# Performance work log

Hardware: AMD Instinct MI355X
Metric: run time of the kernel (lower is better)

The kernel has to match this reference:

```python
import jax, jax.numpy as jnp
import numpy as np

def setup_inputs() -> dict:
    key = jax.random.key(0)
    k1, k2, k3 = jax.random.split(key, 3)
    shape = (2, 2048, 8, 64)  # [n, l, h, d]
    return {
        "q": jax.random.normal(k1, shape, dtype=jnp.float32),
        "k": jax.random.normal(k2, shape, dtype=jnp.float32),
        "v": jax.random.normal(k3, shape, dtype=jnp.float32),
    }

def reference(q, k, v):
    # QK^T: [n, l, s, h]
    qk = jnp.einsum('nlhd,nshd->nlsh', q, k)
    softmax_temp = 1.0 / (q.shape[3] ** 0.5)
    attn = jax.nn.softmax(softmax_temp * qk, axis=2)
    # weighted values: [n, l, h, d]
    return jnp.einsum('nlsh,nshd->nlhd', attn, v)
```

## Files before the change

kernel.cpp:

```cpp
#include <hip/hip_runtime.h>
#include <hip/hip_bf16.h>
#include <math.h>

typedef float floatx4 __attribute__((ext_vector_type(4)));
typedef __bf16 bf16x8 __attribute__((ext_vector_type(8)));

#define SEQ 2048
#define NH 8
#define DH 64
#define NB 2
#define HEADS (NB * NH)
#define HSTRIDE (SEQ * DH)

__device__ __forceinline__ unsigned short f2bf(float x) {
  union { __bf16 b; unsigned short u; } c;
  c.b = (__bf16)x;
  return c.u;
}

__global__ __launch_bounds__(256)
void cvt_kv(const float* __restrict__ k, const float* __restrict__ v,
            unsigned short* __restrict__ kb, unsigned short* __restrict__ vb) {
  __shared__ unsigned short Ts[64][68];
  const int tid  = threadIdx.x;
  const int bx   = blockIdx.x;
  const int ts   = bx & 31;
  const int head = bx >> 5;
  const int n = head >> 3, h = head & 7;

  #pragma unroll
  for (int i = 0; i < 4; ++i) {
    int id = i * 256 + tid;
    int s  = id >> 4;
    int c4 = (id & 15) * 4;
    size_t g = ((size_t)((n * SEQ + ts * 64 + s) * NH + h)) * DH + c4;
    float4 x = *(const float4*)(k + g);
    ushort4 y;
    y.x = f2bf(x.x); y.y = f2bf(x.y); y.z = f2bf(x.z); y.w = f2bf(x.w);
    *(ushort4*)(kb + ((size_t)head * SEQ + ts * 64 + s) * DH + c4) = y;
    float4 xv = *(const float4*)(v + g);
    ushort4 yv;
    yv.x = f2bf(xv.x); yv.y = f2bf(xv.y); yv.z = f2bf(xv.z); yv.w = f2bf(xv.w);
    *(ushort4*)&Ts[s][c4] = yv;
  }
  __syncthreads();
  const int d = tid >> 2;
  const int j = tid & 3;
  size_t ob = ((size_t)head * DH + d) * SEQ + ts * 64 + j * 16;
  #pragma unroll
  for (int c = 0; c < 4; ++c) {
    ushort4 y;
    y.x = Ts[j * 16 + c * 4 + 0][d];
    y.y = Ts[j * 16 + c * 4 + 1][d];
    y.z = Ts[j * 16 + c * 4 + 2][d];
    y.w = Ts[j * 16 + c * 4 + 3][d];
    *(ushort4*)(vb + ob + c * 4) = y;
  }
}

#define SMEM_BYTES 51456

__global__ __launch_bounds__(256, 2)
void attn(const float* __restrict__ q, const unsigned short* __restrict__ kb,
          const unsigned short* __restrict__ vt, float* __restrict__ out) {
  __shared__ __align__(16) char smem[SMEM_BYTES];
  unsigned short (*Pw)[32][72] = (unsigned short (*)[32][72])smem;
  float (*oX)[64][66] = (float (*)[64][66])smem;
  float* lX = (float*)(smem + 3 * 64 * 66 * 4);

  const int tid  = threadIdx.x;
  const int wave = tid >> 6;
  const int lane = tid & 63;
  const int quad = lane >> 4;
  const int l16  = lane & 15;

  const int bx   = blockIdx.x;
  const int head = bx & 15;
  const int qg   = bx >> 4;
  const int n = head >> 3, h = head & 7;

  const unsigned short* kh = kb + (size_t)head * HSTRIDE;
  const unsigned short* vh = vt + (size_t)head * HSTRIDE;

  bf16x8 aq[4][2];
  #pragma unroll
  for (int msub = 0; msub < 4; ++msub)
    #pragma unroll
    for (int f = 0; f < 2; ++f) {
      const float* src = q + ((size_t)((n * SEQ + qg * 64 + msub * 16 + l16) * NH + h)) * DH
                         + f * 32 + quad * 8;
      float4 x0 = *(const float4*)src;
      float4 x1 = *(const float4*)(src + 4);
      union { unsigned short us[8]; bf16x8 v8; } u;
      u.us[0] = f2bf(x0.x); u.us[1] = f2bf(x0.y); u.us[2] = f2bf(x0.z); u.us[3] = f2bf(x0.w);
      u.us[4] = f2bf(x1.x); u.us[5] = f2bf(x1.y); u.us[6] = f2bf(x1.z); u.us[7] = f2bf(x1.w);
      aq[msub][f] = u.v8;
    }

  floatx4 o[4][4];
  float lsum[4][4];
  #pragma unroll
  for (int msub = 0; msub < 4; ++msub) {
    #pragma unroll
    for (int t = 0; t < 4; ++t) o[msub][t] = floatx4{0.f, 0.f, 0.f, 0.f};
    #pragma unroll
    for (int r = 0; r < 4; ++r) lsum[msub][r] = 0.f;
  }

  const float S = 0.125f * 1.4426950408889634f;
  const float C = 12.0f;

  for (int it = 0; it < 8; ++it) {
    const int kbase = (wave * 8 + it) * 64;

    bf16x8 bk[4][2];
    #pragma unroll
    for (int t = 0; t < 4; ++t)
      #pragma unroll
      for (int f = 0; f < 2; ++f)
        bk[t][f] = *(const bf16x8*)(kh + (size_t)(kbase + t * 16 + l16) * DH + f * 32 + quad * 8);
    bf16x8 bv[2][4];
    #pragma unroll
    for (int half = 0; half < 2; ++half)
      #pragma unroll
      for (int t = 0; t < 4; ++t)
        bv[half][t] = *(const bf16x8*)(vh + (size_t)(t * 16 + l16) * SEQ + kbase + half * 32 + quad * 8);

    floatx4 acc[4][4];
    #pragma unroll
    for (int msub = 0; msub < 4; ++msub)
      #pragma unroll
      for (int t = 0; t < 4; ++t) {
        acc[msub][t] = floatx4{0.f, 0.f, 0.f, 0.f};
        #pragma unroll
        for (int f = 0; f < 2; ++f)
          acc[msub][t] = __builtin_amdgcn_mfma_f32_16x16x32_bf16(aq[msub][f], bk[t][f], acc[msub][t], 0, 0, 0);
      }

    #pragma unroll
    for (int mp = 0; mp < 2; ++mp) {
      #pragma unroll
      for (int mi = 0; mi < 2; ++mi) {
        const int msub = mp * 2 + mi;
        #pragma unroll
        for (int t = 0; t < 4; ++t)
          #pragma unroll
          for (int r = 0; r < 4; ++r) {
            float p = __builtin_amdgcn_exp2f(acc[msub][t][r] * S - C);
            lsum[msub][r] += p;
            Pw[wave][mi * 16 + quad * 4 + r][t * 16 + l16] = f2bf(p);
          }
      }
      #pragma unroll
      for (int half = 0; half < 2; ++half)
        #pragma unroll
        for (int mi = 0; mi < 2; ++mi) {
          const int msub = mp * 2 + mi;
          bf16x8 a = *(const bf16x8*)&Pw[wave][mi * 16 + l16][half * 32 + quad * 8];
          #pragma unroll
          for (int t = 0; t < 4; ++t)
            o[msub][t] = __builtin_amdgcn_mfma_f32_16x16x32_bf16(a, bv[half][t], o[msub][t], 0, 0, 0);
        }
    }
  }

  #pragma unroll
  for (int msub = 0; msub < 4; ++msub)
    #pragma unroll
    for (int r = 0; r < 4; ++r) {
      float s = lsum[msub][r];
      #pragma unroll
      for (int d = 1; d < 16; d <<= 1) s += __shfl_xor(s, d, 64);
      lsum[msub][r] = s;
    }

  __syncthreads();
  if (wave != 0) {
    const int w = wave - 1;
    #pragma unroll
    for (int msub = 0; msub < 4; ++msub) {
      #pragma unroll
      for (int t = 0; t < 4; ++t)
        #pragma unroll
        for (int r = 0; r < 4; ++r)
          oX[w][msub * 16 + quad * 4 + r][t * 16 + l16] = o[msub][t][r];
      if (l16 == 0)
        #pragma unroll
        for (int r = 0; r < 4; ++r)
          lX[w * 64 + msub * 16 + quad * 4 + r] = lsum[msub][r];
    }
  }
  __syncthreads();
  if (wave == 0) {
    #pragma unroll
    for (int msub = 0; msub < 4; ++msub)
      #pragma unroll
      for (int r = 0; r < 4; ++r) {
        const int row = msub * 16 + quad * 4 + r;
        float lt = lsum[msub][r] + lX[row] + lX[64 + row] + lX[128 + row];
        float inv = 1.f / lt;
        const int grow = qg * 64 + row;
        size_t ob = ((size_t)((n * SEQ + grow) * NH + h)) * DH + l16;
        #pragma unroll
        for (int t = 0; t < 4; ++t) {
          float val = o[msub][t][r]
                    + oX[0][row][t * 16 + l16]
                    + oX[1][row][t * 16 + l16]
                    + oX[2][row][t * 16 + l16];
          out[ob + t * 16] = val * inv;
        }
      }
  }
}

extern "C" void kernel_launch(void* const* d_in, const int* in_sizes, int n_in,
                              void* d_out, int out_size, void* d_ws, size_t ws_size,
                              hipStream_t stream) {
  const float* q = (const float*)d_in[0];
  const float* k = (const float*)d_in[1];
  const float* v = (const float*)d_in[2];
  float* out = (float*)d_out;
  (void)in_sizes; (void)n_in; (void)out_size; (void)ws_size;

  unsigned short* kb = (unsigned short*)d_ws;
  unsigned short* vb = kb + (size_t)HEADS * HSTRIDE;

  cvt_kv<<<HEADS * (SEQ / 64), 256, 0, stream>>>(k, v, kb, vb);
  attn<<<HEADS * (SEQ / 64), 256, 0, stream>>>(q, kb, vb, out);
}
```

Before: 114.1 us.

## Pre-swizzle K/V into MFMA fragment order and split keys over eight waves

The pack kernel now writes K and transposed V in the exact per-lane MFMA fragment order, so each attention-kernel load becomes one contiguous 16-byte access per lane. The attention block grows to 512 threads (8 waves, 4 key tiles each). QK^T operands are swapped so P comes out transposed, which lets it be written to LDS as packed bf16 pairs, and the row-sum reduction shrinks to two shuffles. The cross-wave combine is done in four 16-row passes using all threads, with float2 output stores. The cost is more LDS passes and barriers in the epilogue, plus register pressure under launch_bounds(512,4).

```diff
diff --git a/kernel.cpp b/kernel.cpp
--- a/kernel.cpp
+++ b/kernel.cpp
@@ -9,64 +9,86 @@
 #define NH 8
 #define DH 64
 #define NB 2
-#define HEADS (NB * NH)
+#define HEADS 16
 #define HSTRIDE (SEQ * DH)
+#define ELEMS (NB * SEQ * NH * DH)
+#define TILE_E (64 * 64)
 
 __device__ __forceinline__ unsigned short f2bf(float x) {
-  union { __bf16 b; unsigned short u; } c;
-  c.b = (__bf16)x;
+  union { __bf16 b; unsigned short u; } c; c.b = (__bf16)x; return c.u;
+}
+__device__ __forceinline__ unsigned int pk2bf(float a, float b) {
+  union { __hip_bfloat162 h2; unsigned int u; } c;
+  c.h2 = __float22bfloat162_rn(make_float2(a, b));
   return c.u;
 }
 
 __global__ __launch_bounds__(256)
-void cvt_kv(const float* __restrict__ k, const float* __restrict__ v,
-            unsigned short* __restrict__ kb, unsigned short* __restrict__ vb) {
+void pack_kv(const float* __restrict__ k, const float* __restrict__ v,
+             unsigned short* __restrict__ kb, unsigned short* __restrict__ vb) {
   __shared__ unsigned short Ts[64][68];
   const int tid  = threadIdx.x;
   const int bx   = blockIdx.x;
-  const int ts   = bx & 31;
+  const int kt   = bx & 31;
   const int head = bx >> 5;
   const int n = head >> 3, h = head & 7;
+
+  #pragma unroll
+  for (int j2 = 0; j2 < 2; ++j2) {
+    int c = j2 * 256 + tid;
+    int t2f = c >> 6, lane = c & 63;
+    int l16 = lane & 15, quad = lane >> 4;
+    int t = t2f >> 1, f = t2f & 1;
+    int s = kt * 64 + t * 16 + l16;
+    const float* src = k + ((size_t)(n * SEQ + s) * NH + h) * DH + f * 32 + quad * 8;
+    float4 a = *(const float4*)src;
+    float4 b = *(const float4*)(src + 4);
+    ushort4 lo, hi;
+    lo.x = f2bf(a.x); lo.y = f2bf(a.y); lo.z = f2bf(a.z); lo.w = f2bf(a.w);
+    hi.x = f2bf(b.x); hi.y = f2bf(b.y); hi.z = f2bf(b.z); hi.w = f2bf(b.w);
+    unsigned short* dst = kb + (size_t)head * HSTRIDE + kt * TILE_E + c * 8;
+    *(ushort4*)dst = lo;
+    *(ushort4*)(dst + 4) = hi;
+  }
 
   #pragma unroll
   for (int i = 0; i < 4; ++i) {
     int id = i * 256 + tid;
     int s  = id >> 4;
     int c4 = (id & 15) * 4;
-    size_t g = ((size_t)((n * SEQ + ts * 64 + s) * NH + h)) * DH + c4;
-    float4 x = *(const float4*)(k + g);
+    size_t g = ((size_t)((n * SEQ + kt * 64 + s) * NH + h)) * DH + c4;
+    float4 x = *(const float4*)(v + g);
     ushort4 y;
     y.x = f2bf(x.x); y.y = f2bf(x.y); y.z = f2bf(x.z); y.w = f2bf(x.w);
-    *(ushort4*)(kb + ((size_t)head * SEQ + ts * 64 + s) * DH + c4) = y;
-    float4 xv = *(const float4*)(v + g);
-    ushort4 yv;
-    yv.x = f2bf(xv.x); yv.y = f2bf(xv.y); yv.z = f2bf(xv.z); yv.w = f2bf(xv.w);
-    *(ushort4*)&Ts[s][c4] = yv;
+    *(ushort4*)&Ts[s][c4] = y;
   }
   __syncthreads();
-  const int d = tid >> 2;
-  const int j = tid & 3;
-  size_t ob = ((size_t)head * DH + d) * SEQ + ts * 64 + j * 16;
-  #pragma unroll
-  for (int c = 0; c < 4; ++c) {
-    ushort4 y;
-    y.x = Ts[j * 16 + c * 4 + 0][d];
-    y.y = Ts[j * 16 + c * 4 + 1][d];
-    y.z = Ts[j * 16 + c * 4 + 2][d];
-    y.w = Ts[j * 16 + c * 4 + 3][d];
-    *(ushort4*)(vb + ob + c * 4) = y;
-  }
-}
-
-#define SMEM_BYTES 51456
-
-__global__ __launch_bounds__(256, 2)
+  #pragma unroll
+  for (int j2 = 0; j2 < 2; ++j2) {
+    int c = j2 * 256 + tid;
+    int h4t = c >> 6, lane = c & 63;
+    int l16 = lane & 15, quad = lane >> 4;
+    int half = h4t >> 2, t = h4t & 3;
+    int d = t * 16 + l16;
+    int s0 = half * 32 + quad * 8;
+    ushort4 lo, hi;
+    lo.x = Ts[s0 + 0][d]; lo.y = Ts[s0 + 1][d]; lo.z = Ts[s0 + 2][d]; lo.w = Ts[s0 + 3][d];
+    hi.x = Ts[s0 + 4][d]; hi.y = Ts[s0 + 5][d]; hi.z = Ts[s0 + 6][d]; hi.w = Ts[s0 + 7][d];
+    unsigned short* dst = vb + (size_t)head * HSTRIDE + kt * TILE_E + c * 8;
+    *(ushort4*)dst = lo;
+    *(ushort4*)(dst + 4) = hi;
+  }
+}
+
+#define SMEM_BYTES 35328
+
+__global__ __launch_bounds__(512, 4)
 void attn(const float* __restrict__ q, const unsigned short* __restrict__ kb,
           const unsigned short* __restrict__ vt, float* __restrict__ out) {
   __shared__ __align__(16) char smem[SMEM_BYTES];
-  unsigned short (*Pw)[32][72] = (unsigned short (*)[32][72])smem;
-  float (*oX)[64][66] = (float (*)[64][66])smem;
-  float* lX = (float*)(smem + 3 * 64 * 66 * 4);
+  unsigned short* PwT = (unsigned short*)smem;
+  float* oM = (float*)smem;
+  float* lM = (float*)(smem + 8 * 16 * 68 * 4);
 
   const int tid  = threadIdx.x;
   const int wave = tid >> 6;
@@ -79,8 +101,8 @@
   const int qg   = bx >> 4;
   const int n = head >> 3, h = head & 7;
 
-  const unsigned short* kh = kb + (size_t)head * HSTRIDE;
-  const unsigned short* vh = vt + (size_t)head * HSTRIDE;
+  const unsigned short* kf = kb + (size_t)head * HSTRIDE;
+  const unsigned short* vf = vt + (size_t)head * HSTRIDE;
 
   bf16x8 aq[4][2];
   #pragma unroll
@@ -91,40 +113,42 @@
                          + f * 32 + quad * 8;
       float4 x0 = *(const float4*)src;
       float4 x1 = *(const float4*)(src + 4);
-      union { unsigned short us[8]; bf16x8 v8; } u;
-      u.us[0] = f2bf(x0.x); u.us[1] = f2bf(x0.y); u.us[2] = f2bf(x0.z); u.us[3] = f2bf(x0.w);
-      u.us[4] = f2bf(x1.x); u.us[5] = f2bf(x1.y); u.us[6] = f2bf(x1.z); u.us[7] = f2bf(x1.w);
+      union { unsigned int u32[4]; bf16x8 v8; } u;
+      u.u32[0] = pk2bf(x0.x, x0.y); u.u32[1] = pk2bf(x0.z, x0.w);
+      u.u32[2] = pk2bf(x1.x, x1.y); u.u32[3] = pk2bf(x1.z, x1.w);
       aq[msub][f] = u.v8;
     }
 
   floatx4 o[4][4];
-  float lsum[4][4];
+  float lsum[4];
   #pragma unroll
   for (int msub = 0; msub < 4; ++msub) {
     #pragma unroll
     for (int t = 0; t < 4; ++t) o[msub][t] = floatx4{0.f, 0.f, 0.f, 0.f};
-    #pragma unroll
-    for (int r = 0; r < 4; ++r) lsum[msub][r] = 0.f;
+    lsum[msub] = 0.f;
   }
 
   const float S = 0.125f * 1.4426950408889634f;
   const float C = 12.0f;
-
-  for (int it = 0; it < 8; ++it) {
-    const int kbase = (wave * 8 + it) * 64;
+  unsigned short* myP = PwT + wave * 16 * 72;
+
+  for (int it = 0; it < 4; ++it) {
+    const int kt = wave * 4 + it;
+    const unsigned short* kbase = kf + kt * TILE_E;
+    const unsigned short* vbase = vf + kt * TILE_E;
 
     bf16x8 bk[4][2];
     #pragma unroll
     for (int t = 0; t < 4; ++t)
       #pragma unroll
       for (int f = 0; f < 2; ++f)
-        bk[t][f] = *(const bf16x8*)(kh + (size_t)(kbase + t * 16 + l16) * DH + f * 32 + quad * 8);
+        bk[t][f] = *(const bf16x8*)(kbase + ((t * 2 + f) * 64 + lane) * 8);
     bf16x8 bv[2][4];
     #pragma unroll
     for (int half = 0; half < 2; ++half)
       #pragma unroll
       for (int t = 0; t < 4; ++t)
-        bv[half][t] = *(const bf16x8*)(vh + (size_t)(t * 16 + l16) * SEQ + kbase + half * 32 + quad * 8);
+        bv[half][t] = *(const bf16x8*)(vbase + ((half * 4 + t) * 64 + lane) * 8);
 
     floatx4 acc[4][4];
     #pragma unroll
@@ -134,82 +158,62 @@
         acc[msub][t] = floatx4{0.f, 0.f, 0.f, 0.f};
         #pragma unroll
         for (int f = 0; f < 2; ++f)
-          acc[msub][t] = __builtin_amdgcn_mfma_f32_16x16x32_bf16(aq[msub][f], bk[t][f], acc[msub][t], 0, 0, 0);
+          acc[msub][t] = __builtin_amdgcn_mfma_f32_16x16x32_bf16(bk[t][f], aq[msub][f], acc[msub][t], 0, 0, 0);
       }
 
     #pragma unroll
-    for (int mp = 0; mp < 2; ++mp) {
-      #pragma unroll
-      for (int mi = 0; mi < 2; ++mi) {
-        const int msub = mp * 2 + mi;
+    for (int msub = 0; msub < 4; ++msub) {
+      #pragma unroll
+      for (int t = 0; t < 4; ++t) {
+        float p0 = __builtin_amdgcn_exp2f(acc[msub][t][0] * S - C);
+        float p1 = __builtin_amdgcn_exp2f(acc[msub][t][1] * S - C);
+        float p2 = __builtin_amdgcn_exp2f(acc[msub][t][2] * S - C);
+        float p3 = __builtin_amdgcn_exp2f(acc[msub][t][3] * S - C);
+        lsum[msub] += (p0 + p1) + (p2 + p3);
+        uint2 pk; pk.x = pk2bf(p0, p1); pk.y = pk2bf(p2, p3);
+        *(uint2*)(myP + l16 * 72 + t * 16 + quad * 4) = pk;
+      }
+      #pragma unroll
+      for (int half = 0; half < 2; ++half) {
+        bf16x8 a = *(const bf16x8*)(myP + l16 * 72 + half * 32 + quad * 8);
         #pragma unroll
         for (int t = 0; t < 4; ++t)
-          #pragma unroll
-          for (int r = 0; r < 4; ++r) {
-            float p = __builtin_amdgcn_exp2f(acc[msub][t][r] * S - C);
-            lsum[msub][r] += p;
-            Pw[wave][mi * 16 + quad * 4 + r][t * 16 + l16] = f2bf(p);
-          }
+          o[msub][t] = __builtin_amdgcn_mfma_f32_16x16x32_bf16(a, bv[half][t], o[msub][t], 0, 0, 0);
       }
-      #pragma unroll
-      for (int half = 0; half < 2; ++half)
-        #pragma unroll
-        for (int mi = 0; mi < 2; ++mi) {
-          const int msub = mp * 2 + mi;
-          bf16x8 a = *(const bf16x8*)&Pw[wave][mi * 16 + l16][half * 32 + quad * 8];
-          #pragma unroll
-          for (int t = 0; t < 4; ++t)
-            o[msub][t] = __builtin_amdgcn_mfma_f32_16x16x32_bf16(a, bv[half][t], o[msub][t], 0, 0, 0);
-        }
     }
   }
 
   #pragma unroll
-  for (int msub = 0; msub < 4; ++msub)
-    #pragma unroll
-    for (int r = 0; r < 4; ++r) {
-      float s = lsum[msub][r];
-      #pragma unroll
-      for (int d = 1; d < 16; d <<= 1) s += __shfl_xor(s, d, 64);
-      lsum[msub][r] = s;
+  for (int msub = 0; msub < 4; ++msub) {
+    float s = lsum[msub];
+    s += __shfl_xor(s, 16, 64);
+    s += __shfl_xor(s, 32, 64);
+    lsum[msub] = s;
+  }
+
+  #pragma unroll
+  for (int p = 0; p < 4; ++p) {
+    __syncthreads();
+    #pragma unroll
+    for (int t = 0; t < 4; ++t)
+      #pragma unroll
+      for (int r = 0; r < 4; ++r)
+        oM[(wave * 16 + quad * 4 + r) * 68 + t * 16 + l16] = o[p][t][r];
+    if (quad == 0) lM[wave * 16 + l16] = lsum[p];
+    __syncthreads();
+    const int idx = tid * 2;
+    const int row = idx >> 6, col = idx & 63;
+    float l = 0.f, v0 = 0.f, v1 = 0.f;
+    #pragma unroll
+    for (int w = 0; w < 8; ++w) {
+      l += lM[w * 16 + row];
+      float2 t2 = *(const float2*)&oM[(w * 16 + row) * 68 + col];
+      v0 += t2.x; v1 += t2.y;
     }
-
-  __syncthreads();
-  if (wave != 0) {
-    const int w = wave - 1;
-    #pragma unroll
-    for (int msub = 0; msub < 4; ++msub) {
-      #pragma unroll
-      for (int t = 0; t < 4; ++t)
-        #pragma unroll
-        for (int r = 0; r < 4; ++r)
-          oX[w][msub * 16 + quad * 4 + r][t * 16 + l16] = o[msub][t][r];
-      if (l16 == 0)
-        #pragma unroll
-        for (int r = 0; r < 4; ++r)
-          lX[w * 64 + msub * 16 + quad * 4 + r] = lsum[msub][r];
-    }
-  }
-  __syncthreads();
-  if (wave == 0) {
-    #pragma unroll
-    for (int msub = 0; msub < 4; ++msub)
-      #pragma unroll
-      for (int r = 0; r < 4; ++r) {
-        const int row = msub * 16 + quad * 4 + r;
-        float lt = lsum[msub][r] + lX[row] + lX[64 + row] + lX[128 + row];
-        float inv = 1.f / lt;
-        const int grow = qg * 64 + row;
-        size_t ob = ((size_t)((n * SEQ + grow) * NH + h)) * DH + l16;
-        #pragma unroll
-        for (int t = 0; t < 4; ++t) {
-          float val = o[msub][t][r]
-                    + oX[0][row][t * 16 + l16]
-                    + oX[1][row][t * 16 + l16]
-                    + oX[2][row][t * 16 + l16];
-          out[ob + t * 16] = val * inv;
-        }
-      }
+    float inv = 1.f / l;
+    const int grow = qg * 64 + p * 16 + row;
+    float2 st; st.x = v0 * inv; st.y = v1 * inv;
+    *(float2*)(out + ((size_t)((n * SEQ + grow) * NH + h)) * DH + col) = st;
   }
 }
 
@@ -225,6 +229,6 @@
   unsigned short* kb = (unsigned short*)d_ws;
   unsigned short* vb = kb + (size_t)HEADS * HSTRIDE;
 
-  cvt_kv<<<HEADS * (SEQ / 64), 256, 0, stream>>>(k, v, kb, vb);
-  attn<<<HEADS * (SEQ / 64), 256, 0, stream>>>(q, kb, vb, out);
-}
+  pack_kv<<<HEADS * (SEQ / 64), 256, 0, stream>>>(k, v, kb, vb);
+  attn<<<HEADS * (SEQ / 64), 512, 0, stream>>>(q, kb, vb, out);
+}
```

Result: slower. 225.8 us (+97.9%).
